# Kernel optimization log

Measured on AMD Instinct MI355X. Metric: run time of the kernel, lower is better.

## Reference

```python
import jax, jax.numpy as jnp
import numpy as np

N_NODES = 50000
N_EDGES = 800000
IN_F = 256
OUT_F = 64
N_HEADS = 8
LRELU_SLOPE = 0.2


def setup_inputs() -> dict:
    key = jax.random.key(0)
    ks = jax.random.split(key, 6)
    x = jax.random.normal(ks[0], (N_NODES, IN_F), dtype=jnp.float32)
    src = jax.random.randint(ks[1], (N_EDGES,), 0, N_NODES, dtype=jnp.int32)
    dst = jax.random.randint(ks[2], (N_EDGES,), 0, N_NODES, dtype=jnp.int32)
    M_values = jax.random.uniform(ks[3], (N_EDGES,), dtype=jnp.float32)
    # xavier_uniform-ish scale (gain=1.414)
    wscale = 1.414 * np.sqrt(6.0 / (IN_F + OUT_F))
    W = jax.random.uniform(ks[4], (N_HEADS, IN_F, OUT_F), dtype=jnp.float32,
                           minval=-wscale, maxval=wscale)
    ascale = 1.414 * np.sqrt(6.0 / (OUT_F + 1))
    a = jax.random.uniform(ks[5], (N_HEADS, 2, OUT_F), dtype=jnp.float32,
                           minval=-ascale, maxval=ascale)
    return {"x": x, "src": src, "dst": dst, "M_values": M_values, "W": W, "a": a}


def reference(x, src, dst, M_values, W, a):
    # x: [N, Fin]; src/dst: [E]; M_values: [E] (edge-aligned mask/weights)
    # W: [H, Fin, Fout]; a: [H, 2, Fout] (a[:,0]=a_self, a[:,1]=a_neighs)
    N = x.shape[0]
    outs = []
    for hidx in range(W.shape[0]):  # small fixed head count
        h = x @ W[hidx]                       # [N, Fout]
        a_self = h @ a[hidx, 0]               # [N]
        a_neigh = h @ a[hidx, 1]              # [N]
        e = jax.nn.leaky_relu(a_self[src] + a_neigh[dst], LRELU_SLOPE) * M_values  # [E]
        exp_e = jnp.exp(e)
        denom = jax.ops.segment_sum(exp_e, dst, num_segments=N)   # [N]
        att = exp_e / (denom[dst] + 1e-16)                        # [E]
        h_prime = jax.ops.segment_sum(att[:, None] * h[src], dst, num_segments=N)  # [N, Fout]
        outs.append(jax.nn.elu(h_prime))      # concat=True -> elu per head
    return jnp.concatenate(outs, axis=1)       # [N, H*Fout]
```

## Files before the change

kernel.cpp:

```cpp
#include <hip/hip_runtime.h>
#include <math.h>

#define N_NODES 50000
#define N_EDGES 800000
#define IN_F 256
#define OUT_F 64
#define N_HEADS 8
#define SLOPE 0.2f
#define MAXDEG 64

typedef __attribute__((ext_vector_type(8))) __bf16 bf16x8;
typedef __attribute__((ext_vector_type(4))) __bf16 bf16x4;
typedef __attribute__((ext_vector_type(4))) float floatx4;
typedef __attribute__((ext_vector_type(4))) float f32x4;
typedef __attribute__((ext_vector_type(2))) int i32x2;
typedef __attribute__((ext_vector_type(2))) unsigned int u32x2;
typedef __attribute__((ext_vector_type(8))) char schar8;

#define FW_BLOCKS (512 + 3125)
__global__ __launch_bounds__(256) void fill_wcast_kernel(
        const float* __restrict__ W, __bf16* __restrict__ Wt,
        const int* __restrict__ src, const int* __restrict__ dst,
        const float* __restrict__ M, int* __restrict__ cursor,
        i32x2* __restrict__ csr_b) {
    const int b = blockIdx.x;
    if (b < 512) {
        int i = b * 256 + threadIdx.x;
        int n = i & (OUT_F - 1);
        int k = (i >> 6) & (IN_F - 1);
        int h = i >> 14;
        Wt[((size_t)h * OUT_F + n) * IN_F + k] = (__bf16)W[i];
        return;
    }
    int e = (b - 512) * 256 + threadIdx.x;
    int d = dst[e];
    int r = atomicAdd(&cursor[d], 1);
    if (r < MAXDEG) {
        i32x2 v;
        v.x = src[e];
        v.y = __float_as_int(M[e] * 1.44269504f);
        __builtin_nontemporal_store(v, csr_b + ((size_t)d << 6) + r);
    }
}

#define XPAD 264
__global__ __launch_bounds__(256) void mfma_gemm_kernel(const float* __restrict__ x,
                                                        const __bf16* __restrict__ Wt,
                                                        const float* __restrict__ a,
                                                        unsigned char* __restrict__ hb,
                                                        float2* __restrict__ asc,
                                                        float* __restrict__ a_neigh) {
    __shared__ __bf16 xs[32][XPAD];
    const int warp = threadIdx.x >> 6;
    const int tile = blockIdx.x;
    const int n0 = tile * 32;
    const int lane = threadIdx.x & 63;
    const int l15 = lane & 15;
    const int quad = lane >> 4;
    const int h0 = warp * 2;

#pragma unroll
    for (int i = 0; i < 8; i++) {
        int c4 = i * 256 + threadIdx.x;
        int row = c4 >> 6;
        int col = (c4 & 63) * 4;
        int node = n0 + row;
        node = (node < N_NODES) ? node : (N_NODES - 1);
        f32x4 v = __builtin_nontemporal_load((const f32x4*)x + (size_t)node * 64 + (c4 & 63));
        bf16x4 o;
        o[0] = (__bf16)v[0]; o[1] = (__bf16)v[1]; o[2] = (__bf16)v[2]; o[3] = (__bf16)v[3];
        *(bf16x4*)&xs[row][col] = o;
    }
    __syncthreads();

    floatx4 acc[2][2][4];
#pragma unroll
    for (int hh = 0; hh < 2; hh++)
#pragma unroll
        for (int i = 0; i < 2; i++)
#pragma unroll
            for (int c = 0; c < 4; c++) acc[hh][i][c] = floatx4{0.f, 0.f, 0.f, 0.f};

    const __bf16* wb0 = Wt + ((size_t)h0 * OUT_F + l15) * IN_F + quad * 8;
    const __bf16* wb1 = wb0 + (size_t)OUT_F * IN_F;

#pragma unroll
    for (int k0 = 0; k0 < IN_F; k0 += 32) {
        bf16x8 a0 = *(const bf16x8*)&xs[l15][k0 + quad * 8];
        bf16x8 a1 = *(const bf16x8*)&xs[l15 + 16][k0 + quad * 8];
#pragma unroll
        for (int c = 0; c < 4; c++) {
            bf16x8 b0 = *(const bf16x8*)(wb0 + (size_t)c * 16 * IN_F + k0);
            acc[0][0][c] = __builtin_amdgcn_mfma_f32_16x16x32_bf16(a0, b0, acc[0][0][c], 0, 0, 0);
            acc[0][1][c] = __builtin_amdgcn_mfma_f32_16x16x32_bf16(a1, b0, acc[0][1][c], 0, 0, 0);
            bf16x8 b1 = *(const bf16x8*)(wb1 + (size_t)c * 16 * IN_F + k0);
            acc[1][0][c] = __builtin_amdgcn_mfma_f32_16x16x32_bf16(a0, b1, acc[1][0][c], 0, 0, 0);
            acc[1][1][c] = __builtin_amdgcn_mfma_f32_16x16x32_bf16(a1, b1, acc[1][1][c], 0, 0, 0);
        }
    }

    __syncthreads();
    char* myc = (char*)xs + warp * (32 * OUT_F);

#pragma unroll
    for (int hh = 0; hh < 2; hh++) {
        const int head = h0 + hh;
        float av0[4], av1[4];
#pragma unroll
        for (int c = 0; c < 4; c++) {
            av0[c] = a[head * 2 * OUT_F + c * 16 + l15];
            av1[c] = a[head * 2 * OUT_F + OUT_F + c * 16 + l15];
        }
#pragma unroll
        for (int i = 0; i < 2; i++) {
#pragma unroll
            for (int reg = 0; reg < 4; reg++) {
                float ps = 0.f, pn = 0.f, rm = 0.f;
#pragma unroll
                for (int c = 0; c < 4; c++) {
                    float v = acc[hh][i][c][reg];
                    ps = fmaf(v, av0[c], ps);
                    pn = fmaf(v, av1[c], pn);
                    rm = fmaxf(rm, fabsf(v));
                }
#pragma unroll
                for (int off = 1; off < 16; off <<= 1) {
                    ps += __shfl_xor(ps, off, 64);
                    pn += __shfl_xor(pn, off, 64);
                    rm = fmaxf(rm, __shfl_xor(rm, off, 64));
                }
                const float inv = (rm > 0.f) ? 127.f / rm : 0.f;
                const int rowoff = (i * 16 + quad * 4 + reg) * OUT_F;
#pragma unroll
                for (int c = 0; c < 4; c++) {
                    float q = rintf(acc[hh][i][c][reg] * inv);
                    q = fminf(fmaxf(q, -127.f), 127.f);
                    myc[rowoff + c * 16 + l15] = (char)((int)q + 128);
                }
                int node = n0 + i * 16 + quad * 4 + reg;
                if (l15 == 0 && node < N_NODES) {
                    asc[node * N_HEADS + head] = make_float2(ps, rm * (1.f / 127.f));
                    a_neigh[node * N_HEADS + head] = pn;
                }
            }
        }
#pragma unroll
        for (int pass = 0; pass < 4; pass++) {
            int row = pass * 8 + (lane >> 3);
            int node = n0 + row;
            schar8 v = *(const schar8*)&myc[row * OUT_F + (lane & 7) * 8];
            if (node < N_NODES)
                *(schar8*)(hb + ((size_t)(node * N_HEADS + head) << 6) + (lane & 7) * 8) = v;
        }
    }
}

__global__ __launch_bounds__(512) void agg_kernel(const unsigned char* __restrict__ hb,
                                                  const float2* __restrict__ asc,
                                                  const float* __restrict__ a_neigh,
                                                  const int* __restrict__ deg,
                                                  const i32x2* __restrict__ csr_b,
                                                  float* __restrict__ out) {
    int n = blockIdx.x * 8 + (threadIdx.x >> 6);
    const int lane = threadIdx.x & 63;
    const int head = lane >> 3;

    int d = deg[n];
    d = (d < MAXDEG) ? d : MAXDEG;
    float* ob = &out[((size_t)n << 9) + (lane << 3)];
    if (d == 0) {
        f32x4 z = {0.f, 0.f, 0.f, 0.f};
        *(f32x4*)(ob) = z;
        *(f32x4*)(ob + 4) = z;
        return;
    }
    const int dm1 = d - 1;
    const float an = a_neigh[(n << 3) + head];
    const char* hbB = (const char*)hb;
    const char* ascB = (const char*)asc;
    const unsigned int loff = (unsigned)lane << 3;
    const unsigned int hoff = (unsigned)head << 3;
    const i32x2* cp = csr_b + ((size_t)n << 6);

    float facc[8];
#pragma unroll
    for (int k = 0; k < 8; k++) facc[k] = 0.f;
    float den = 0.f, sacc = 0.f;

    auto edge = [&](const i32x2& sm, const float2& a2, const u32x2& hv) {
        float s = a2.x + an;
        float e_ = fmaxf(s, SLOPE * s);
        const float w_ = exp2f(e_ * __int_as_float(sm.y));
        const float ws = w_ * a2.y;
        den += w_;
        sacc += ws;
        facc[0] = fmaf(ws, (float)(hv.x & 0xffu), facc[0]);
        facc[1] = fmaf(ws, (float)((hv.x >> 8) & 0xffu), facc[1]);
        facc[2] = fmaf(ws, (float)((hv.x >> 16) & 0xffu), facc[2]);
        facc[3] = fmaf(ws, (float)(hv.x >> 24), facc[3]);
        facc[4] = fmaf(ws, (float)(hv.y & 0xffu), facc[4]);
        facc[5] = fmaf(ws, (float)((hv.y >> 8) & 0xffu), facc[5]);
        facc[6] = fmaf(ws, (float)((hv.y >> 16) & 0xffu), facc[6]);
        facc[7] = fmaf(ws, (float)(hv.y >> 24), facc[7]);
    };

    i32x2 smP = cp[0];
    float2 aP = *(const float2*)(ascB + (((unsigned)smP.x << 6) | hoff));
    u32x2 hvP = *(const u32x2*)(hbB + (((unsigned)smP.x << 9) | loff));

    int j = 0;
    for (; j + 2 <= d; j += 2) {
        i32x2 smQ = cp[j + 1];
        float2 aQ = *(const float2*)(ascB + (((unsigned)smQ.x << 6) | hoff));
        u32x2 hvQ = *(const u32x2*)(hbB + (((unsigned)smQ.x << 9) | loff));
        edge(smP, aP, hvP);
        int i2 = (j + 2 < d) ? (j + 2) : dm1;
        smP = cp[i2];
        aP = *(const float2*)(ascB + (((unsigned)smP.x << 6) | hoff));
        hvP = *(const u32x2*)(hbB + (((unsigned)smP.x << 9) | loff));
        edge(smQ, aQ, hvQ);
    }
    if (j < d) edge(smP, aP, hvP);

    const float inv = 1.f / (den + 1e-16f);
    float r[8];
#pragma unroll
    for (int k = 0; k < 8; k++) {
        float v = fmaf(-128.f, sacc, facc[k]) * inv;
        r[k] = (v > 0.f) ? v : expm1f(v);
    }
    *(float4*)(ob)     = make_float4(r[0], r[1], r[2], r[3]);
    *(float4*)(ob + 4) = make_float4(r[4], r[5], r[6], r[7]);
}

extern "C" void kernel_launch(void* const* d_in, const int* in_sizes, int n_in,
                              void* d_out, int out_size, void* d_ws, size_t ws_size,
                              hipStream_t stream) {
    const float* x   = (const float*)d_in[0];
    const int*   src = (const int*)d_in[1];
    const int*   dst = (const int*)d_in[2];
    const float* M   = (const float*)d_in[3];
    const float* W   = (const float*)d_in[4];
    const float* a   = (const float*)d_in[5];
    float* out = (float*)d_out;

    char* p = (char*)d_ws;
    auto alloc = [&](size_t bytes) {
        char* r = p;
        p += (bytes + 255) & ~(size_t)255;
        return r;
    };
    unsigned char* hb = (unsigned char*)alloc((size_t)N_NODES * N_HEADS * OUT_F);
    float2* asc     = (float2*)alloc(sizeof(float2) * N_NODES * N_HEADS);
    float*  a_neigh = (float*)alloc(sizeof(float) * N_NODES * N_HEADS);
    int*    cursor  = (int*)alloc(sizeof(int) * N_NODES);
    i32x2*  csr_b   = (i32x2*)alloc(sizeof(i32x2) * (size_t)N_NODES * MAXDEG);
    __bf16* Wt      = (__bf16*)alloc(sizeof(__bf16) * N_HEADS * IN_F * OUT_F);

    hipMemsetAsync(cursor, 0, sizeof(int) * N_NODES, stream);
    fill_wcast_kernel<<<FW_BLOCKS, 256, 0, stream>>>(W, Wt, src, dst, M,
                                                     cursor, csr_b);

    mfma_gemm_kernel<<<1563, 256, 0, stream>>>(x, Wt, a, hb, asc, a_neigh);

    agg_kernel<<<6250, 512, 0, stream>>>(hb, asc, a_neigh, cursor, csr_b, out);
}
```

Baseline: 369.3 us.

## Fuse CSR fill with GEMM in one interleaved launch and replace memset

Merges the edge-bucketing fill and the MFMA projection GEMM into a single kernel whose blocks alternate between the two roles, so the atomic-heavy scatter overlaps with compute. The memset of the degree cursor is folded into the weight-cast kernel. This removes a launch and a serialization point. The trade-off is that fill blocks now reserve the GEMM's shared memory, which can lower their occupancy.

```diff
diff --git a/kernel.cpp b/kernel.cpp
--- a/kernel.cpp
+++ b/kernel.cpp
@@ -17,12 +17,12 @@
 typedef __attribute__((ext_vector_type(2))) unsigned int u32x2;
 typedef __attribute__((ext_vector_type(8))) char schar8;
 
-#define FW_BLOCKS (512 + 3125)
-__global__ __launch_bounds__(256) void fill_wcast_kernel(
-        const float* __restrict__ W, __bf16* __restrict__ Wt,
-        const int* __restrict__ src, const int* __restrict__ dst,
-        const float* __restrict__ M, int* __restrict__ cursor,
-        i32x2* __restrict__ csr_b) {
+#define XPAD 264
+
+#define INIT_BLOCKS (512 + 196)
+__global__ __launch_bounds__(256) void init_kernel(const float* __restrict__ W,
+                                                   __bf16* __restrict__ Wt,
+                                                   int* __restrict__ cursor) {
     const int b = blockIdx.x;
     if (b < 512) {
         int i = b * 256 + threadIdx.x;
@@ -30,30 +30,19 @@
         int k = (i >> 6) & (IN_F - 1);
         int h = i >> 14;
         Wt[((size_t)h * OUT_F + n) * IN_F + k] = (__bf16)W[i];
-        return;
-    }
-    int e = (b - 512) * 256 + threadIdx.x;
-    int d = dst[e];
-    int r = atomicAdd(&cursor[d], 1);
-    if (r < MAXDEG) {
-        i32x2 v;
-        v.x = src[e];
-        v.y = __float_as_int(M[e] * 1.44269504f);
-        __builtin_nontemporal_store(v, csr_b + ((size_t)d << 6) + r);
-    }
-}
-
-#define XPAD 264
-__global__ __launch_bounds__(256) void mfma_gemm_kernel(const float* __restrict__ x,
-                                                        const __bf16* __restrict__ Wt,
-                                                        const float* __restrict__ a,
-                                                        unsigned char* __restrict__ hb,
-                                                        float2* __restrict__ asc,
-                                                        float* __restrict__ a_neigh) {
-    __shared__ __bf16 xs[32][XPAD];
+    } else {
+        int i = (b - 512) * 256 + threadIdx.x;
+        if (i < N_NODES) cursor[i] = 0;
+    }
+}
+
+__device__ __forceinline__ void gemm_tile(
+        int g, __bf16 (*xs)[XPAD],
+        const float* __restrict__ x, const __bf16* __restrict__ Wt,
+        const float* __restrict__ a, unsigned char* __restrict__ hb,
+        float2* __restrict__ asc, float* __restrict__ a_neigh) {
     const int warp = threadIdx.x >> 6;
-    const int tile = blockIdx.x;
-    const int n0 = tile * 32;
+    const int n0 = g * 32;
     const int lane = threadIdx.x & 63;
     const int l15 = lane & 15;
     const int quad = lane >> 4;
@@ -152,6 +141,32 @@
             if (node < N_NODES)
                 *(schar8*)(hb + ((size_t)(node * N_HEADS + head) << 6) + (lane & 7) * 8) = v;
         }
+    }
+}
+
+#define FG_BLOCKS 4688
+__global__ __launch_bounds__(256) void fill_gemm_kernel(
+        const int* __restrict__ src, const int* __restrict__ dst,
+        const float* __restrict__ M, int* __restrict__ cursor,
+        i32x2* __restrict__ csr_b,
+        const float* __restrict__ x, const __bf16* __restrict__ Wt,
+        const float* __restrict__ a, unsigned char* __restrict__ hb,
+        float2* __restrict__ asc, float* __restrict__ a_neigh) {
+    __shared__ __bf16 xs[32][XPAD];
+    const int b = blockIdx.x;
+    if ((b % 3) == 0) {
+        gemm_tile(b / 3, xs, x, Wt, a, hb, asc, a_neigh);
+        return;
+    }
+    int fb = b - (b + 2) / 3;
+    int e = fb * 256 + threadIdx.x;
+    int d = dst[e];
+    int r = atomicAdd(&cursor[d], 1);
+    if (r < MAXDEG) {
+        i32x2 v;
+        v.x = src[e];
+        v.y = __float_as_int(M[e] * 1.44269504f);
+        __builtin_nontemporal_store(v, csr_b + ((size_t)d << 6) + r);
     }
 }
 
@@ -257,11 +272,10 @@
     i32x2*  csr_b   = (i32x2*)alloc(sizeof(i32x2) * (size_t)N_NODES * MAXDEG);
     __bf16* Wt      = (__bf16*)alloc(sizeof(__bf16) * N_HEADS * IN_F * OUT_F);
 
-    hipMemsetAsync(cursor, 0, sizeof(int) * N_NODES, stream);
-    fill_wcast_kernel<<<FW_BLOCKS, 256, 0, stream>>>(W, Wt, src, dst, M,
-                                                     cursor, csr_b);
-
-    mfma_gemm_kernel<<<1563, 256, 0, stream>>>(x, Wt, a, hb, asc, a_neigh);
+    init_kernel<<<INIT_BLOCKS, 256, 0, stream>>>(W, Wt, cursor);
+
+    fill_gemm_kernel<<<FG_BLOCKS, 256, 0, stream>>>(src, dst, M, cursor, csr_b,
+                                                    x, Wt, a, hb, asc, a_neigh);
 
     agg_kernel<<<6250, 512, 0, stream>>>(hb, asc, a_neigh, cursor, csr_b, out);
 }
```

New measurement: 338.5 us. 1.09x faster.
